# Kernel optimization log

Hardware: AMD Instinct MI355X
Metric: run time of the kernel (lower is better)

Reference implementation:

```python
import jax, jax.numpy as jnp
import numpy as np

N_NODES = 50000
N_EDGES = 800000
NDIM_IN = 64
EDIMS = 64
NDIM_OUT = 128


def setup_inputs() -> dict:
    key = jax.random.key(0)
    k = jax.random.split(key, 8)
    nfeats = jax.random.normal(k[0], (N_NODES, NDIM_IN), dtype=jnp.float32)
    efeats = jax.random.normal(k[1], (N_EDGES, EDIMS), dtype=jnp.float32)
    # Linear weights stored as [in, out]; scaled for stable activations.
    W_msg = jax.random.normal(k[2], (NDIM_IN + EDIMS, NDIM_OUT), dtype=jnp.float32) * 0.05
    b_msg = jax.random.normal(k[3], (NDIM_OUT,), dtype=jnp.float32) * 0.05
    W_apply = jax.random.normal(k[4], (NDIM_IN + NDIM_OUT, NDIM_OUT), dtype=jnp.float32) * 0.05
    b_apply = jax.random.normal(k[5], (NDIM_OUT,), dtype=jnp.float32) * 0.05
    src = jax.random.randint(k[6], (N_EDGES,), 0, N_NODES, dtype=jnp.int64)
    dst = jax.random.randint(k[7], (N_EDGES,), 0, N_NODES, dtype=jnp.int64)
    return {
        "nfeats": nfeats,
        "efeats": efeats,
        "W_msg": W_msg,
        "b_msg": b_msg,
        "W_apply": W_apply,
        "b_apply": b_apply,
        "src": src,
        "dst": dst,
    }


def reference(nfeats, efeats, W_msg, b_msg, W_apply, b_apply, src, dst):
    # message: per-edge gather src node feats, concat with edge feats, linear+relu
    msg_in = jnp.concatenate([nfeats[src], efeats], axis=1)          # [E, ndim_in+edims]
    m = jax.nn.relu(msg_in @ W_msg + b_msg)                           # [E, ndim_out]
    # aggregate: sum messages into destination nodes
    h_neigh = jax.ops.segment_sum(m, dst, num_segments=nfeats.shape[0])  # [N, ndim_out]
    # update: concat original node feats with aggregated messages, linear+relu
    out = jax.nn.relu(jnp.concatenate([nfeats, h_neigh], axis=1) @ W_apply + b_apply)
    return out
```

## Files before the change

### kernel.cpp

```cpp
#include <hip/hip_runtime.h>
#include <hip/hip_bf16.h>

#define N_NODES  50000
#define N_EDGES  800000
#define NDIM_IN  64
#define EDIMS    64
#define NDIM_OUT 128

typedef __bf16 bf16;
typedef bf16  bf16x8 __attribute__((ext_vector_type(8)));
typedef float f32x4  __attribute__((ext_vector_type(4)));

__device__ __forceinline__ bool detect_f32(const void* nfeats) {
    const unsigned short* w = (const unsigned short*)nfeats;
    for (int i = 0; i < 64; i += 2) {
        const int e = (w[i] >> 7) & 0xFF;
        if (e < 100 || e > 134) return true;
    }
    return false;
}
__device__ __forceinline__ bool detect_i64(const int* p) {
    for (int i = 1; i < 64; i += 2) if (p[i] != 0) return false;
    return true;
}

__device__ __forceinline__ bf16x8 load8(const void* p, long off, bool f32) {
    if (f32) {
        const float* q = (const float*)p + off;
        const f32x4 a = *(const f32x4*)q;
        const f32x4 b = *(const f32x4*)(q + 4);
        bf16x8 r;
        #pragma unroll
        for (int u = 0; u < 4; ++u) { r[u] = (bf16)a[u]; r[4 + u] = (bf16)b[u]; }
        return r;
    }
    return *(const bf16x8*)((const bf16*)p + off);
}
__device__ __forceinline__ float loadf(const void* p, int i, bool f32) {
    return f32 ? ((const float*)p)[i] : (float)((const bf16*)p)[i];
}
__device__ __forceinline__ void storef(void* p, int i, float v, bool f32) {
    if (f32) ((float*)p)[i] = v; else ((bf16*)p)[i] = (bf16)v;
}

__global__ __launch_bounds__(256) void hist_kernel(const int* __restrict__ dst,
                                                   int* __restrict__ cnt) {
    __shared__ int s_ish;
    if (threadIdx.x == 0) s_ish = detect_i64(dst) ? 1 : 0;
    __syncthreads();
    const int ish = s_ish;
    const int stride = gridDim.x * blockDim.x;
    for (int e = blockIdx.x * blockDim.x + threadIdx.x; e < N_EDGES; e += stride)
        atomicAdd(&cnt[dst[e << ish]], 1);
}

__global__ __launch_bounds__(1024) void scan_kernel(int* __restrict__ cnt,
                                                    int* __restrict__ row_ptr) {
    __shared__ int sw[16];
    const int t    = threadIdx.x;
    const int lane = t & 63;
    const int w    = t >> 6;
    const int base = t * 52;

    int sum = 0;
    #pragma unroll
    for (int j = 0; j < 13; ++j) {
        const int4 q = *(const int4*)(cnt + base + j * 4);
        sum += q.x + q.y + q.z + q.w;
    }
    int s = sum;
    #pragma unroll
    for (int off = 1; off < 64; off <<= 1) {
        const int u = __shfl_up(s, off, 64);
        if (lane >= off) s += u;
    }
    if (lane == 63) sw[w] = s;
    __syncthreads();
    if (t < 16) {
        int x = sw[t];
        #pragma unroll
        for (int off = 1; off < 16; off <<= 1) {
            const int u = __shfl_up(x, off, 16);
            if ((t & 15) >= off) x += u;
        }
        sw[t] = x;
    }
    __syncthreads();
    int run = (w > 0 ? sw[w - 1] : 0) + (s - sum);
    #pragma unroll
    for (int j = 0; j < 13; ++j) {
        const int4 q = *(const int4*)(cnt + base + j * 4);
        int4 r;
        r.x = run; run += q.x;
        r.y = run; run += q.y;
        r.z = run; run += q.z;
        r.w = run; run += q.w;
        *(int4*)(row_ptr + base + j * 4) = r;
        *(int4*)(cnt     + base + j * 4) = r;
    }
}

__global__ __launch_bounds__(256) void gather_kernel(
    const void* __restrict__ nfeats,
    const void* __restrict__ efeats,
    const int*  __restrict__ src,
    const int*  __restrict__ dst,
    int*        __restrict__ cursor,
    bf16*       __restrict__ A)
{
    __shared__ int s_flags;
    const int tid = threadIdx.x;
    if (tid == 0)
        s_flags = (detect_f32(nfeats) ? 1 : 0) | (detect_i64(dst) ? 2 : 0);
    __syncthreads();
    const bool f32 = (s_flags & 1) != 0;
    const int  ish = (s_flags & 2) ? 1 : 0;

    const int lane = tid & 63;
    const int wave = tid >> 6;
    const int c    = lane & 3;
    const int ei   = lane >> 2;

    const int ngroups = N_EDGES / 16;
    const int nw      = gridDim.x * 4;
    for (int g = blockIdx.x * 4 + wave; g < ngroups; g += nw) {
        const int e = g * 16 + ei;
        int pos = 0;
        if (c == 0) pos = atomicAdd(&cursor[dst[(long)e << ish]], 1);
        pos = __shfl(pos, lane & ~3, 64);
        const int s_ = src[(long)e << ish];

        const void* bsrc = (c < 2) ? nfeats : efeats;
        const int   row  = (c < 2) ? s_ : e;
        const int   ko   = (c & 1) * 32;
        bf16* outp = A + (size_t)pos * 128 + c * 32;
        #pragma unroll
        for (int j = 0; j < 4; ++j) {
            const bf16x8 v = load8(bsrc, (long)row * 64 + ko + j * 8, f32);
            *(bf16x8*)(outp + j * 8) = v;
        }
    }
}

__global__ __launch_bounds__(256) void msg_agg_dense(
    const void* __restrict__ nfeats,
    const bf16* __restrict__ A,
    const void* __restrict__ W_msg,
    const void* __restrict__ b_msg,
    const int*  __restrict__ row_ptr,
    float*      __restrict__ h_neigh)
{
    __shared__ bf16 sWT[128 * 136];
    __shared__ int s_flags;

    const int tid = threadIdx.x;
    if (tid == 0) s_flags = detect_f32(nfeats) ? 1 : 0;
    __syncthreads();
    const bool f32 = (s_flags & 1) != 0;

    #pragma unroll
    for (int it = 0; it < 8; ++it) {
        const int task = it * 256 + tid;
        const int k = task >> 4;
        const int c = task & 15;
        const bf16x8 w = load8(W_msg, k * 128 + c * 8, f32);
        #pragma unroll
        for (int u = 0; u < 8; ++u) sWT[(c * 8 + u) * 136 + k] = w[u];
    }
    __syncthreads();

    const int wave = tid >> 6;
    const int lane = tid & 63;
    const int m    = lane & 15;
    const int quad = lane >> 4;

    float bias[8];
    #pragma unroll
    for (int t = 0; t < 8; ++t) bias[t] = loadf(b_msg, t * 16 + m, f32);

    const int wstride = gridDim.x * 4;
    for (int v = blockIdx.x * 4 + wave; v < N_NODES; v += wstride) {
        const int beg = row_ptr[v];
        const int deg = row_ptr[v + 1] - beg;

        float hacc[8] = {0.f, 0.f, 0.f, 0.f, 0.f, 0.f, 0.f, 0.f};

        for (int T = 0; T * 16 < deg; ++T) {
            const int r0 = T * 16;
            const int sl = (r0 + m < deg) ? (beg + r0 + m) : beg;
            const bf16* ap = A + (size_t)sl * 128 + quad * 8;

            bf16x8 a[4];
            #pragma unroll
            for (int kb = 0; kb < 4; ++kb)
                a[kb] = *(const bf16x8*)(ap + kb * 32);

            #pragma unroll
            for (int t = 0; t < 8; ++t) {
                f32x4 acc = {0.f, 0.f, 0.f, 0.f};
                const bf16* bp = sWT + (t * 16 + m) * 136 + quad * 8;
                #pragma unroll
                for (int kb = 0; kb < 4; ++kb)
                    acc = __builtin_amdgcn_mfma_f32_16x16x32_bf16(
                              a[kb], *(const bf16x8*)(bp + kb * 32), acc, 0, 0, 0);
                float part = 0.f;
                #pragma unroll
                for (int i = 0; i < 4; ++i) {
                    float val = acc[i] + bias[t];
                    val = val > 0.f ? val : 0.f;
                    if (r0 + quad * 4 + i < deg) part += val;
                }
                hacc[t] += part;
            }
        }

        #pragma unroll
        for (int t = 0; t < 8; ++t) {
            float s = hacc[t];
            s += __shfl_xor(s, 16, 64);
            s += __shfl_xor(s, 32, 64);
            hacc[t] = s;
        }

        const float lo = quad < 2 ? (quad == 0 ? hacc[0] : hacc[1])
                                  : (quad == 2 ? hacc[2] : hacc[3]);
        const float hi = quad < 2 ? (quad == 0 ? hacc[4] : hacc[5])
                                  : (quad == 2 ? hacc[6] : hacc[7]);
        h_neigh[v * 128 + lane]      = lo;
        h_neigh[v * 128 + 64 + lane] = hi;
    }
}

__global__ __launch_bounds__(256) void scatter_kernel(const int* __restrict__ src,
                                                      const int* __restrict__ dst,
                                                      int* __restrict__ cursor,
                                                      int* __restrict__ eid,
                                                      int* __restrict__ srcs) {
    __shared__ int s_ish;
    if (threadIdx.x == 0) s_ish = detect_i64(dst) ? 1 : 0;
    __syncthreads();
    const int ish = s_ish;
    const int stride = gridDim.x * blockDim.x;
    for (int e = blockIdx.x * blockDim.x + threadIdx.x; e < N_EDGES; e += stride) {
        const int d = dst[(long)e << ish];
        const int pos = atomicAdd(&cursor[d], 1);
        eid[pos]  = e;
        srcs[pos] = src[(long)e << ish];
    }
}

__global__ __launch_bounds__(256) void msg_agg_kernel(
    const void* __restrict__ nfeats,
    const void* __restrict__ efeats,
    const void* __restrict__ W_msg,
    const void* __restrict__ b_msg,
    const int*  __restrict__ row_ptr,
    const int*  __restrict__ eid,
    const int*  __restrict__ srcs,
    float*      __restrict__ h_neigh)
{
    __shared__ bf16 sWT[128 * 136];
    __shared__ int s_flags;

    const int tid = threadIdx.x;
    if (tid == 0) s_flags = detect_f32(nfeats) ? 1 : 0;
    __syncthreads();
    const bool f32 = (s_flags & 1) != 0;

    #pragma unroll
    for (int it = 0; it < 8; ++it) {
        const int task = it * 256 + tid;
        const int k = task >> 4;
        const int c = task & 15;
        const bf16x8 w = load8(W_msg, k * 128 + c * 8, f32);
        #pragma unroll
        for (int u = 0; u < 8; ++u) sWT[(c * 8 + u) * 136 + k] = w[u];
    }
    __syncthreads();

    const int wave = tid >> 6;
    const int lane = tid & 63;
    const int m    = lane & 15;
    const int quad = lane >> 4;

    float bias[8];
    #pragma unroll
    for (int t = 0; t < 8; ++t) bias[t] = loadf(b_msg, t * 16 + m, f32);

    const int wstride = gridDim.x * 4;
    for (int v = blockIdx.x * 4 + wave; v < N_NODES; v += wstride) {
        const int beg = row_ptr[v];
        const int deg = row_ptr[v + 1] - beg;

        float hacc[8] = {0.f, 0.f, 0.f, 0.f, 0.f, 0.f, 0.f, 0.f};

        for (int T = 0; T * 16 < deg; ++T) {
            const int r0 = T * 16;
            const int sl = (r0 + m < deg) ? (beg + r0 + m) : beg;
            const int s  = srcs[sl];
            const int e  = eid[sl];

            bf16x8 a[4];
            a[0] = load8(nfeats, (long)s * 64 +      quad * 8, f32);
            a[1] = load8(nfeats, (long)s * 64 + 32 + quad * 8, f32);
            a[2] = load8(efeats, (long)e * 64 +      quad * 8, f32);
            a[3] = load8(efeats, (long)e * 64 + 32 + quad * 8, f32);

            #pragma unroll
            for (int t = 0; t < 8; ++t) {
                f32x4 acc = {0.f, 0.f, 0.f, 0.f};
                const bf16* bp = sWT + (t * 16 + m) * 136 + quad * 8;
                #pragma unroll
                for (int kb = 0; kb < 4; ++kb)
                    acc = __builtin_amdgcn_mfma_f32_16x16x32_bf16(
                              a[kb], *(const bf16x8*)(bp + kb * 32), acc, 0, 0, 0);
                float part = 0.f;
                #pragma unroll
                for (int i = 0; i < 4; ++i) {
                    float val = acc[i] + bias[t];
                    val = val > 0.f ? val : 0.f;
                    if (r0 + quad * 4 + i < deg) part += val;
                }
                hacc[t] += part;
            }
        }

        #pragma unroll
        for (int t = 0; t < 8; ++t) {
            float s = hacc[t];
            s += __shfl_xor(s, 16, 64);
            s += __shfl_xor(s, 32, 64);
            hacc[t] = s;
        }

        const float lo = quad < 2 ? (quad == 0 ? hacc[0] : hacc[1])
                                  : (quad == 2 ? hacc[2] : hacc[3]);
        const float hi = quad < 2 ? (quad == 0 ? hacc[4] : hacc[5])
                                  : (quad == 2 ? hacc[6] : hacc[7]);
        h_neigh[v * 128 + lane]      = lo;
        h_neigh[v * 128 + 64 + lane] = hi;
    }
}

__global__ __launch_bounds__(256) void edge_msg_kernel(
    const void* __restrict__ nfeats,
    const void* __restrict__ efeats,
    const void* __restrict__ W_msg,
    const void* __restrict__ b_msg,
    const int*  __restrict__ src,
    const int*  __restrict__ dst,
    float*      __restrict__ h_neigh)
{
    __shared__ bf16 sWT[128 * 136];
    __shared__ int s_flags;

    const int tid = threadIdx.x;
    if (tid == 0)
        s_flags = (detect_f32(nfeats) ? 1 : 0) | (detect_i64(dst) ? 2 : 0);
    __syncthreads();
    const bool f32 = (s_flags & 1) != 0;
    const int  ish = (s_flags & 2) ? 1 : 0;

    #pragma unroll
    for (int it = 0; it < 8; ++it) {
        const int task = it * 256 + tid;
        const int k = task >> 4;
        const int c = task & 15;
        const bf16x8 w = load8(W_msg, k * 128 + c * 8, f32);
        #pragma unroll
        for (int u = 0; u < 8; ++u) sWT[(c * 8 + u) * 136 + k] = w[u];
    }
    __syncthreads();

    const int wave = tid >> 6;
    const int lane = tid & 63;
    const int m    = lane & 15;
    const int quad = lane >> 4;

    const int nchunks = N_EDGES / 64;
    for (int chunk = blockIdx.x; chunk < nchunks; chunk += gridDim.x) {
        const int ebase = chunk * 64 + wave * 16;
        const int e_m   = ebase + m;
        const int s     = src[(long)e_m << ish];

        bf16x8 a[4];
        a[0] = load8(nfeats, (long)s   * 64 +      quad * 8, f32);
        a[1] = load8(nfeats, (long)s   * 64 + 32 + quad * 8, f32);
        a[2] = load8(efeats, (long)e_m * 64 +      quad * 8, f32);
        a[3] = load8(efeats, (long)e_m * 64 + 32 + quad * 8, f32);

        int drow[4];
        #pragma unroll
        for (int i = 0; i < 4; ++i)
            drow[i] = dst[(long)(ebase + quad * 4 + i) << ish] * 128;

        #pragma unroll
        for (int t = 0; t < 8; ++t) {
            f32x4 acc = {0.f, 0.f, 0.f, 0.f};
            const bf16* bp = sWT + (t * 16 + m) * 136 + quad * 8;
            #pragma unroll
            for (int kb = 0; kb < 4; ++kb)
                acc = __builtin_amdgcn_mfma_f32_16x16x32_bf16(
                          a[kb], *(const bf16x8*)(bp + kb * 32), acc, 0, 0, 0);
            const int   n    = t * 16 + m;
            const float bias = loadf(b_msg, n, f32);
            #pragma unroll
            for (int i = 0; i < 4; ++i) {
                float v = acc[i] + bias;
                v = v > 0.f ? v : 0.f;
                unsafeAtomicAdd(h_neigh + drow[i] + n, v);
            }
        }
    }
}

__global__ __launch_bounds__(256) void apply_kernel(
    const void*  __restrict__ nfeats,
    const float* __restrict__ h_neigh,
    const void*  __restrict__ W_apply,
    const void*  __restrict__ b_apply,
    void*        __restrict__ out)
{
    __shared__ bf16 sWT[128 * 200];
    __shared__ int s_flags;

    const int tid = threadIdx.x;
    if (tid == 0) s_flags = detect_f32(nfeats) ? 1 : 0;
    __syncthreads();
    const bool f32 = (s_flags & 1) != 0;

    #pragma unroll
    for (int it = 0; it < 12; ++it) {
        const int task = it * 256 + tid;
        const int k = task >> 4;
        const int c = task & 15;
        const bf16x8 w = load8(W_apply, k * 128 + c * 8, f32);
        #pragma unroll
        for (int u = 0; u < 8; ++u) sWT[(c * 8 + u) * 200 + k] = w[u];
    }
    __syncthreads();

    const int wave = tid >> 6;
    const int lane = tid & 63;
    const int m    = lane & 15;
    const int quad = lane >> 4;

    const int nchunks = (N_NODES + 63) / 64;
    for (int chunk = blockIdx.x; chunk < nchunks; chunk += gridDim.x) {
        const int nbase = chunk * 64 + wave * 16;
        const int nm  = nbase + m;
        const int nmc = nm < N_NODES ? nm : N_NODES - 1;

        bf16x8 a[6];
        a[0] = load8(nfeats, (long)nmc * 64 +      quad * 8, f32);
        a[1] = load8(nfeats, (long)nmc * 64 + 32 + quad * 8, f32);
        #pragma unroll
        for (int kb = 0; kb < 4; ++kb) {
            const float* hp = h_neigh + (size_t)nmc * 128 + kb * 32 + quad * 8;
            const f32x4 p = *(const f32x4*)(hp);
            const f32x4 q = *(const f32x4*)(hp + 4);
            bf16x8 r;
            #pragma unroll
            for (int u = 0; u < 4; ++u) { r[u] = (bf16)p[u]; r[4 + u] = (bf16)q[u]; }
            a[2 + kb] = r;
        }

        #pragma unroll
        for (int t = 0; t < 8; ++t) {
            f32x4 acc = {0.f, 0.f, 0.f, 0.f};
            const bf16* bp = sWT + (t * 16 + m) * 200 + quad * 8;
            #pragma unroll
            for (int kb = 0; kb < 6; ++kb)
                acc = __builtin_amdgcn_mfma_f32_16x16x32_bf16(
                          a[kb], *(const bf16x8*)(bp + kb * 32), acc, 0, 0, 0);
            const int   n    = t * 16 + m;
            const float bias = loadf(b_apply, n, f32);
            #pragma unroll
            for (int i = 0; i < 4; ++i) {
                const int row = nbase + quad * 4 + i;
                if (row < N_NODES) {
                    float v = acc[i] + bias;
                    v = v > 0.f ? v : 0.f;
                    storef(out, row * 128 + n, v, f32);
                }
            }
        }
    }
}

extern "C" void kernel_launch(void* const* d_in, const int* in_sizes, int n_in,
                              void* d_out, int out_size, void* d_ws, size_t ws_size,
                              hipStream_t stream) {
    const void* nfeats  = d_in[0];
    const void* efeats  = d_in[1];
    const void* W_msg   = d_in[2];
    const void* b_msg   = d_in[3];
    const void* W_apply = d_in[4];
    const void* b_apply = d_in[5];
    const int*  src     = (const int*)d_in[6];
    const int*  dst     = (const int*)d_in[7];

    float* h_neigh = (float*)d_ws;

    const size_t SZ_PAD     = 213248;
    const size_t OFF_ROWPTR = 25600000;
    const size_t OFF_CNT    = OFF_ROWPTR + SZ_PAD;
    const size_t OFF_A      = OFF_CNT + SZ_PAD;
    const size_t NEED_DENSE = OFF_A + (size_t)N_EDGES * 128 * 2;
    const size_t OFF_EID    = OFF_A;
    const size_t OFF_SRCS   = OFF_EID + 3200000;
    const size_t NEED_CSR   = OFF_SRCS + 3200000;

    int* row_ptr = (int*)((char*)d_ws + OFF_ROWPTR);
    int* cnt     = (int*)((char*)d_ws + OFF_CNT);

    if (ws_size >= NEED_DENSE) {
        bf16* A = (bf16*)((char*)d_ws + OFF_A);
        hipMemsetAsync(cnt, 0, (size_t)53248 * sizeof(int), stream);
        hist_kernel<<<1024, 256, 0, stream>>>(dst, cnt);
        scan_kernel<<<1, 1024, 0, stream>>>(cnt, row_ptr);
        gather_kernel<<<1024, 256, 0, stream>>>(nfeats, efeats, src, dst, cnt, A);
        msg_agg_dense<<<1024, 256, 0, stream>>>(nfeats, A, W_msg, b_msg,
                                                row_ptr, h_neigh);
    } else if (ws_size >= NEED_CSR) {
        int* eid  = (int*)((char*)d_ws + OFF_EID);
        int* srcs = (int*)((char*)d_ws + OFF_SRCS);
        hipMemsetAsync(cnt, 0, (size_t)53248 * sizeof(int), stream);
        hist_kernel<<<1024, 256, 0, stream>>>(dst, cnt);
        scan_kernel<<<1, 1024, 0, stream>>>(cnt, row_ptr);
        scatter_kernel<<<1024, 256, 0, stream>>>(src, dst, cnt, eid, srcs);
        msg_agg_kernel<<<1024, 256, 0, stream>>>(nfeats, efeats, W_msg, b_msg,
                                                 row_ptr, eid, srcs, h_neigh);
    } else {
        hipMemsetAsync(h_neigh, 0, (size_t)N_NODES * NDIM_OUT * sizeof(float), stream);
        edge_msg_kernel<<<768, 256, 0, stream>>>(nfeats, efeats, W_msg, b_msg,
                                                 src, dst, h_neigh);
    }

    apply_kernel<<<782, 256, 0, stream>>>(nfeats, h_neigh, W_apply, b_apply, d_out);
}
```

Measured before the change: 691.8 us.

## Pre-convert node features to bf16 table and widen gather to 16 lanes per edge

Adds a kernel that converts nfeats to a bf16 table once, so the per-edge gather reads half the bytes for the src-node part. The gather now uses 16 lanes per edge, each moving one 16-byte chunk, with twice as many blocks, for more coalesced access and more memory parallelism. Weight transposes into LDS now write whole vectors instead of scattered scalar stores, and several index computations are widened to 64-bit. It costs an extra kernel launch and about 6.4 MB of extra workspace, and the table path is used only when the workspace is large enough.

Measured after the change: 608.1 us. 1.14x faster.

```diff
diff --git a/kernel.cpp b/kernel.cpp
--- a/kernel.cpp
+++ b/kernel.cpp
@@ -36,11 +36,23 @@
     }
     return *(const bf16x8*)((const bf16*)p + off);
 }
-__device__ __forceinline__ float loadf(const void* p, int i, bool f32) {
+__device__ __forceinline__ float loadf(const void* p, long i, bool f32) {
     return f32 ? ((const float*)p)[i] : (float)((const bf16*)p)[i];
 }
-__device__ __forceinline__ void storef(void* p, int i, float v, bool f32) {
+__device__ __forceinline__ void storef(void* p, long i, float v, bool f32) {
     if (f32) ((float*)p)[i] = v; else ((bf16*)p)[i] = (bf16)v;
+}
+
+__global__ __launch_bounds__(256) void nf2bf_kernel(const void* __restrict__ nfeats,
+                                                    bf16* __restrict__ tbl) {
+    __shared__ int s_flags;
+    if (threadIdx.x == 0) s_flags = detect_f32(nfeats) ? 1 : 0;
+    __syncthreads();
+    const bool f32 = (s_flags & 1) != 0;
+    const int total  = N_NODES * 64 / 8;
+    const int stride = gridDim.x * blockDim.x;
+    for (int i = blockIdx.x * blockDim.x + threadIdx.x; i < total; i += stride)
+        *(bf16x8*)(tbl + (size_t)i * 8) = load8(nfeats, (long)i * 8, f32);
 }
 
 __global__ __launch_bounds__(256) void hist_kernel(const int* __restrict__ dst,
@@ -51,7 +63,7 @@
     const int ish = s_ish;
     const int stride = gridDim.x * blockDim.x;
     for (int e = blockIdx.x * blockDim.x + threadIdx.x; e < N_EDGES; e += stride)
-        atomicAdd(&cnt[dst[e << ish]], 1);
+        atomicAdd(&cnt[dst[(long)e << ish]], 1);
 }
 
 __global__ __launch_bounds__(1024) void scan_kernel(int* __restrict__ cnt,
@@ -101,44 +113,44 @@
 }
 
 __global__ __launch_bounds__(256) void gather_kernel(
-    const void* __restrict__ nfeats,
+    const void* __restrict__ nfsrc,
     const void* __restrict__ efeats,
     const int*  __restrict__ src,
     const int*  __restrict__ dst,
     int*        __restrict__ cursor,
-    bf16*       __restrict__ A)
+    bf16*       __restrict__ A,
+    const int   tbl)
 {
     __shared__ int s_flags;
     const int tid = threadIdx.x;
     if (tid == 0)
-        s_flags = (detect_f32(nfeats) ? 1 : 0) | (detect_i64(dst) ? 2 : 0);
+        s_flags = (detect_f32(efeats) ? 1 : 0) | (detect_i64(dst) ? 2 : 0);
     __syncthreads();
     const bool f32 = (s_flags & 1) != 0;
     const int  ish = (s_flags & 2) ? 1 : 0;
 
     const int lane = tid & 63;
     const int wave = tid >> 6;
-    const int c    = lane & 3;
-    const int ei   = lane >> 2;
-
-    const int ngroups = N_EDGES / 16;
+    const int q    = lane & 15;
+    const int ei   = lane >> 4;
+
+    const int ngroups = N_EDGES / 4;
     const int nw      = gridDim.x * 4;
     for (int g = blockIdx.x * 4 + wave; g < ngroups; g += nw) {
-        const int e = g * 16 + ei;
+        const int e = g * 4 + ei;
         int pos = 0;
-        if (c == 0) pos = atomicAdd(&cursor[dst[(long)e << ish]], 1);
-        pos = __shfl(pos, lane & ~3, 64);
-        const int s_ = src[(long)e << ish];
-
-        const void* bsrc = (c < 2) ? nfeats : efeats;
-        const int   row  = (c < 2) ? s_ : e;
-        const int   ko   = (c & 1) * 32;
-        bf16* outp = A + (size_t)pos * 128 + c * 32;
-        #pragma unroll
-        for (int j = 0; j < 4; ++j) {
-            const bf16x8 v = load8(bsrc, (long)row * 64 + ko + j * 8, f32);
-            *(bf16x8*)(outp + j * 8) = v;
-        }
+        if (q == 0) pos = atomicAdd(&cursor[dst[(long)e << ish]], 1);
+        pos = __shfl(pos, lane & 48, 64);
+
+        bf16x8 v;
+        if (q < 8) {
+            const int s_ = src[(long)e << ish];
+            v = tbl ? *(const bf16x8*)((const bf16*)nfsrc + (size_t)s_ * 64 + q * 8)
+                    : load8(nfsrc, (long)s_ * 64 + q * 8, f32);
+        } else {
+            v = load8(efeats, (long)e * 64 + (q - 8) * 8, f32);
+        }
+        *(bf16x8*)(A + (size_t)pos * 128 + q * 8) = v;
     }
 }
 
@@ -161,11 +173,13 @@
     #pragma unroll
     for (int it = 0; it < 8; ++it) {
         const int task = it * 256 + tid;
-        const int k = task >> 4;
-        const int c = task & 15;
-        const bf16x8 w = load8(W_msg, k * 128 + c * 8, f32);
-        #pragma unroll
-        for (int u = 0; u < 8; ++u) sWT[(c * 8 + u) * 136 + k] = w[u];
+        const int n    = task & 127;
+        const int kb8  = task >> 7;
+        bf16x8 w;
+        #pragma unroll
+        for (int j = 0; j < 8; ++j)
+            w[j] = (bf16)loadf(W_msg, (long)(kb8 * 8 + j) * 128 + n, f32);
+        *(bf16x8*)(sWT + n * 136 + kb8 * 8) = w;
     }
     __syncthreads();
 
@@ -226,8 +240,8 @@
                                   : (quad == 2 ? hacc[2] : hacc[3]);
         const float hi = quad < 2 ? (quad == 0 ? hacc[4] : hacc[5])
                                   : (quad == 2 ? hacc[6] : hacc[7]);
-        h_neigh[v * 128 + lane]      = lo;
-        h_neigh[v * 128 + 64 + lane] = hi;
+        h_neigh[(size_t)v * 128 + lane]      = lo;
+        h_neigh[(size_t)v * 128 + 64 + lane] = hi;
     }
 }
 
@@ -272,7 +286,7 @@
         const int task = it * 256 + tid;
         const int k = task >> 4;
         const int c = task & 15;
-        const bf16x8 w = load8(W_msg, k * 128 + c * 8, f32);
+        const bf16x8 w = load8(W_msg, (long)k * 128 + c * 8, f32);
         #pragma unroll
         for (int u = 0; u < 8; ++u) sWT[(c * 8 + u) * 136 + k] = w[u];
     }
@@ -337,8 +351,8 @@
                                   : (quad == 2 ? hacc[2] : hacc[3]);
         const float hi = quad < 2 ? (quad == 0 ? hacc[4] : hacc[5])
                                   : (quad == 2 ? hacc[6] : hacc[7]);
-        h_neigh[v * 128 + lane]      = lo;
-        h_neigh[v * 128 + 64 + lane] = hi;
+        h_neigh[(size_t)v * 128 + lane]      = lo;
+        h_neigh[(size_t)v * 128 + 64 + lane] = hi;
     }
 }
 
@@ -366,7 +380,7 @@
         const int task = it * 256 + tid;
         const int k = task >> 4;
         const int c = task & 15;
-        const bf16x8 w = load8(W_msg, k * 128 + c * 8, f32);
+        const bf16x8 w = load8(W_msg, (long)k * 128 + c * 8, f32);
         #pragma unroll
         for (int u = 0; u < 8; ++u) sWT[(c * 8 + u) * 136 + k] = w[u];
     }
@@ -432,11 +446,13 @@
     #pragma unroll
     for (int it = 0; it < 12; ++it) {
         const int task = it * 256 + tid;
-        const int k = task >> 4;
-        const int c = task & 15;
-        const bf16x8 w = load8(W_apply, k * 128 + c * 8, f32);
-        #pragma unroll
-        for (int u = 0; u < 8; ++u) sWT[(c * 8 + u) * 200 + k] = w[u];
+        const int n    = task & 127;
+        const int kb8  = task >> 7;
+        bf16x8 w;
+        #pragma unroll
+        for (int j = 0; j < 8; ++j)
+            w[j] = (bf16)loadf(W_apply, (long)(kb8 * 8 + j) * 128 + n, f32);
+        *(bf16x8*)(sWT + n * 200 + kb8 * 8) = w;
     }
     __syncthreads();
 
@@ -481,7 +497,7 @@
                 if (row < N_NODES) {
                     float v = acc[i] + bias;
                     v = v > 0.f ? v : 0.f;
-                    storef(out, row * 128 + n, v, f32);
+                    storef(out, (long)row * 128 + n, v, f32);
                 }
             }
         }
@@ -506,7 +522,10 @@
     const size_t OFF_ROWPTR = 25600000;
     const size_t OFF_CNT    = OFF_ROWPTR + SZ_PAD;
     const size_t OFF_A      = OFF_CNT + SZ_PAD;
-    const size_t NEED_DENSE = OFF_A + (size_t)N_EDGES * 128 * 2;
+    const size_t SZ_A       = (size_t)N_EDGES * 128 * 2;
+    const size_t OFF_NF     = OFF_A + SZ_A;
+    const size_t NEED_DENSE = OFF_A + SZ_A;
+    const size_t NEED_TBL   = OFF_NF + (size_t)N_NODES * 64 * 2;
     const size_t OFF_EID    = OFF_A;
     const size_t OFF_SRCS   = OFF_EID + 3200000;
     const size_t NEED_CSR   = OFF_SRCS + 3200000;
@@ -515,11 +534,16 @@
     int* cnt     = (int*)((char*)d_ws + OFF_CNT);
 
     if (ws_size >= NEED_DENSE) {
-        bf16* A = (bf16*)((char*)d_ws + OFF_A);
+        bf16* A   = (bf16*)((char*)d_ws + OFF_A);
+        const int tbl = (ws_size >= NEED_TBL) ? 1 : 0;
+        bf16* nft = (bf16*)((char*)d_ws + OFF_NF);
+
         hipMemsetAsync(cnt, 0, (size_t)53248 * sizeof(int), stream);
+        if (tbl) nf2bf_kernel<<<1563, 256, 0, stream>>>(nfeats, nft);
         hist_kernel<<<1024, 256, 0, stream>>>(dst, cnt);
         scan_kernel<<<1, 1024, 0, stream>>>(cnt, row_ptr);
-        gather_kernel<<<1024, 256, 0, stream>>>(nfeats, efeats, src, dst, cnt, A);
+        gather_kernel<<<2048, 256, 0, stream>>>(tbl ? (const void*)nft : nfeats,
+                                                efeats, src, dst, cnt, A, tbl);
         msg_agg_dense<<<1024, 256, 0, stream>>>(nfeats, A, W_msg, b_msg,
                                                 row_ptr, h_neigh);
     } else if (ws_size >= NEED_CSR) {
```
